# Performance work log

Measured on AMD Instinct MI355X. Metric: run time of the kernel, lower is better.

The kernel has to match this reference:

```python
import jax, jax.numpy as jnp
import numpy as np

N = 1_000_000
D = 128
S = 16384


def setup_inputs() -> dict:
    key = jax.random.key(0)
    k_x, k_idx, k_w, k_b = jax.random.split(key, 4)
    x = jax.random.normal(k_x, (N, D), dtype=jnp.float32)
    index = jnp.sort(jax.random.randint(k_idx, (N,), 0, S, dtype=jnp.int64))
    # single plain Linear layer of PyG MLP([D, D], plain_last=True)
    lim = 1.0 / np.sqrt(D)
    W = jax.random.uniform(k_w, (D, D), dtype=jnp.float32, minval=-lim, maxval=lim)
    b = jax.random.uniform(k_b, (D,), dtype=jnp.float32, minval=-lim, maxval=lim)
    return {"x": x, "W": W, "b": b, "index": index, "num_segments": S}


def reference(x, W, b, index, num_segments):
    # att = MLP(x): single plain linear layer (no activation, plain_last=True)
    att = x @ W.T + b  # [N, D]
    # segment softmax over nodes within each graph, per channel (PyG softmax)
    seg_max = jax.ops.segment_max(att, index, num_segments=num_segments)  # [S, D]
    e = jnp.exp(att - seg_max[index])  # [N, D]
    seg_sum = jax.ops.segment_sum(e, index, num_segments=num_segments)  # [S, D]
    att = e / (seg_sum[index] + 1e-16)  # [N, D]
    # attention-weighted global add pool
    return jax.ops.segment_sum(x * att, index, num_segments=num_segments)  # [S, D]
```

## Files before the change

### kernel.cpp

```cpp
#include <hip/hip_runtime.h>
#include <hip/hip_bf16.h>

#define SEGS   16384
#define DCH    128
#define CHUNK  32
#define SEGPB  4
#define FPITCH 132
#define XHBLK  520
#define LOG2E  1.4426950408889634f

using f32x4  = __attribute__((ext_vector_type(4))) float;
using bf16x8 = __attribute__((ext_vector_type(8))) short;
using u32x2  = __attribute__((ext_vector_type(2))) unsigned int;
using u32x4  = __attribute__((ext_vector_type(4))) unsigned int;

__device__ __forceinline__ float u2f(unsigned int u) { return __uint_as_float(u); }
__device__ __forceinline__ unsigned int f2u(float f) { return __float_as_uint(f); }

__global__ void setup_kernel(const float* __restrict__ W,
                             const int* __restrict__ index, int N,
                             unsigned short* __restrict__ WfH,
                             int* __restrict__ seg_start) {
  int i = blockIdx.x * blockDim.x + threadIdx.x;
  if (i < DCH * DCH) {
    int n = i >> 7, k = i & 127;
    float w = W[i] * LOG2E;
    unsigned int u = f2u(w);
    unsigned int r = (u + 0x7FFFu + ((u >> 16) & 1)) >> 16;
    int kt    = k >> 5;
    int ntile = n >> 4;
    int lane  = (n & 15) + 16 * ((k >> 3) & 3);
    int j     = k & 7;
    int dst = ((kt * 8 + ntile) * 64 + lane) * 8 + j;
    WfH[dst] = (unsigned short)r;
  } else if (i < DCH * DCH + SEGS + 1) {
    int s = i - DCH * DCH;
    int lo = 0, hi = N;
    while (lo < hi) {
      int mid = (lo + hi) >> 1;
      if (index[mid] < s) lo = mid + 1; else hi = mid;
    }
    seg_start[s] = lo;
  }
}

__global__ __launch_bounds__(256) void pool_kernel(
    const float* __restrict__ x, const float* __restrict__ bias,
    const int* __restrict__ seg_start,
    const u32x4* __restrict__ WfH,
    float* __restrict__ out) {
  __shared__ unsigned short xh[8 * XHBLK];
  __shared__ float          xf[CHUNK * FPITCH];

  const int t    = threadIdx.x;
  const int wv   = t >> 6;
  const int lane = t & 63;
  const int cl   = lane & 15;
  const int g    = lane >> 4;
  const int k31  = t & 31;
  const int lrow = t >> 5;
  const int lcol = k31 << 2;

  const int xh_base = 1040 * (k31 >> 3) + 8 * lrow + 128 * ((k31 >> 1) & 3) + 4 * (k31 & 1);
  const int xf_base = lrow * FPITCH + lcol;
  const int frag_base = lane * 8;
  const int ex_base   = g * 4 * FPITCH + wv * 32 + cl;

  u32x4 bh[4][2];
#pragma unroll
  for (int kt = 0; kt < 4; ++kt)
#pragma unroll
    for (int nt = 0; nt < 2; ++nt) {
      int off = (kt * 8 + (wv * 2 + nt)) * 64 + lane;
      bh[kt][nt] = WfH[off];
    }

  const float bc0 = bias[wv * 32 + cl]      * LOG2E;
  const float bc1 = bias[wv * 32 + 16 + cl] * LOG2E;

  const int s0   = blockIdx.x * SEGPB;
  const int sEnd = s0 + SEGPB;

  for (int es = s0; es < sEnd; ++es) {
    if (seg_start[es + 1] == seg_start[es] && lane < 16) {
      out[(size_t)es * DCH + wv * 32 + cl]      = 0.f;
      out[(size_t)es * DCH + wv * 32 + 16 + cl] = 0.f;
    }
  }

  int s = s0;
  while (s < sEnd && seg_start[s + 1] == seg_start[s]) ++s;
  if (s >= sEnd) return;

  int c0  = 0;
  int len = seg_start[s + 1] - seg_start[s];
  int cnt = (len < CHUNK) ? len : CHUNK;

  f32x4 pv[4];
  {
    const int base = seg_start[s];
#pragma unroll
    for (int p = 0; p < 4; ++p) {
      int lr = lrow + p * 8;
      f32x4 v = {0.f, 0.f, 0.f, 0.f};
      if (lr < cnt) v = *(const f32x4*)(x + (size_t)(base + lr) * DCH + lcol);
      pv[p] = v;
    }
  }

  float den[2] = {0.f, 0.f};
  float num[2] = {0.f, 0.f};

  while (true) {
    int ns = s, nc0 = c0 + CHUNK;
    if (nc0 >= len) {
      nc0 = 0; ns = s + 1;
      while (ns < sEnd && seg_start[ns + 1] == seg_start[ns]) ++ns;
    }
    const bool have_next = (ns < sEnd);
    int nlen = 0, ncnt = 0, nbase = 0;
    if (have_next) {
      nbase = seg_start[ns] + nc0;
      nlen  = seg_start[ns + 1] - seg_start[ns];
      ncnt  = nlen - nc0; if (ncnt > CHUNK) ncnt = CHUNK;
    }

#pragma unroll
    for (int p = 0; p < 4; ++p) {
      f32x4 v = pv[p];
      unsigned int u0 = f2u(v[0]), u1 = f2u(v[1]), u2 = f2u(v[2]), u3 = f2u(v[3]);
      u32x2 H = { (u1 & 0xFFFF0000u) | (u0 >> 16),
                  (u3 & 0xFFFF0000u) | (u2 >> 16) };
      *(u32x2*)&xh[xh_base + (p >> 1) * XHBLK + (p & 1) * 64] = H;
      *(f32x4*)&xf[xf_base + p * 8 * FPITCH] = v;
    }

    if (have_next) {
#pragma unroll
      for (int p = 0; p < 4; ++p) {
        int lr = lrow + p * 8;
        f32x4 v = {0.f, 0.f, 0.f, 0.f};
        if (lr < ncnt) v = *(const f32x4*)(x + (size_t)(nbase + lr) * DCH + lcol);
        pv[p] = v;
      }
    }

    asm volatile("s_waitcnt lgkmcnt(0)" ::: "memory");
    __builtin_amdgcn_sched_barrier(0);
    __builtin_amdgcn_s_barrier();
    __builtin_amdgcn_sched_barrier(0);

    f32x4 Cf[2][2];
#pragma unroll
    for (int mt = 0; mt < 2; ++mt) {
      Cf[mt][0] = (f32x4){bc0, bc0, bc0, bc0};
      Cf[mt][1] = (f32x4){bc1, bc1, bc1, bc1};
    }

#pragma unroll
    for (int kt = 0; kt < 4; ++kt) {
      u32x4 ah[2];
#pragma unroll
      for (int mt = 0; mt < 2; ++mt)
        ah[mt] = *(const u32x4*)&xh[frag_base + (2 * kt + mt) * XHBLK];
#pragma unroll
      for (int mt = 0; mt < 2; ++mt)
#pragma unroll
        for (int nt = 0; nt < 2; ++nt) {
          bf16x8 A = __builtin_bit_cast(bf16x8, ah[mt]);
          bf16x8 B = __builtin_bit_cast(bf16x8, bh[kt][nt]);
          Cf[mt][nt] = __builtin_amdgcn_mfma_f32_16x16x32_bf16(A, B, Cf[mt][nt], 0, 0, 0);
        }
    }

#pragma unroll
    for (int nt = 0; nt < 2; ++nt) {
#pragma unroll
      for (int mt = 0; mt < 2; ++mt)
#pragma unroll
        for (int r = 0; r < 4; ++r) {
          const int row = mt * 16 + g * 4 + r;
          float p = __builtin_amdgcn_exp2f(Cf[mt][nt][r]);
          p = (row < cnt) ? p : 0.f;
          float xv = xf[ex_base + (mt * 16 + r) * FPITCH + nt * 16];
          den[nt] += p;
          num[nt] += p * xv;
        }
    }

    if (c0 + CHUNK >= len) {
#pragma unroll
      for (int nt = 0; nt < 2; ++nt) {
        float l = den[nt], a = num[nt];
        l += __shfl_xor(l, 16); l += __shfl_xor(l, 32);
        a += __shfl_xor(a, 16); a += __shfl_xor(a, 32);
        if (lane < 16)
          out[(size_t)s * DCH + wv * 32 + nt * 16 + cl] = a / (l + 1e-16f);
        den[nt] = 0.f; num[nt] = 0.f;
      }
      if (!have_next) break;
      s = ns; len = nlen; c0 = 0;
    } else {
      c0 = nc0;
    }
    cnt = ncnt;

    asm volatile("s_waitcnt lgkmcnt(0)" ::: "memory");
    __builtin_amdgcn_sched_barrier(0);
    __builtin_amdgcn_s_barrier();
    __builtin_amdgcn_sched_barrier(0);
  }
}

extern "C" void kernel_launch(void* const* d_in, const int* in_sizes, int n_in,
                              void* d_out, int out_size, void* d_ws, size_t ws_size,
                              hipStream_t stream) {
  const float* x    = (const float*)d_in[0];
  const float* W    = (const float*)d_in[1];
  const float* bias = (const float*)d_in[2];
  const int*   idx  = (const int*)d_in[3];
  const int N = in_sizes[0] / DCH;

  unsigned short* WfH = (unsigned short*)d_ws;
  int* seg = (int*)(WfH + DCH * DCH);

  int setup_threads = DCH * DCH + SEGS + 1;
  setup_kernel<<<(setup_threads + 255) / 256, 256, 0, stream>>>(W, idx, N, WfH, seg);
  pool_kernel<<<SEGS / SEGPB, 256, 0, stream>>>(x, bias, seg,
                                                (const u32x4*)WfH,
                                                (float*)d_out);
}
```

Before: 125.1 us.

## Deepen x prefetch to two chunks ahead and double segments per block

Register prefetch of x chunks moves from one chunk ahead to two, using ping-pong buffers pvA/pvB. Each chunk's load is issued two iterations before it is consumed, which gives more time to hide global memory latency. SEGPB also doubles from 4 to 8, so the grid has half as many blocks, each handling more segments. The cost is higher register pressure and fewer blocks, which may reduce occupancy and parallelism.

After: 129.9 us. +3.8%, slower.

```diff
diff --git a/kernel.cpp b/kernel.cpp
--- a/kernel.cpp
+++ b/kernel.cpp
@@ -4,7 +4,7 @@
 #define SEGS   16384
 #define DCH    128
 #define CHUNK  32
-#define SEGPB  4
+#define SEGPB  8
 #define FPITCH 132
 #define XHBLK  520
 #define LOG2E  1.4426950408889634f
@@ -92,13 +92,13 @@
   while (s < sEnd && seg_start[s + 1] == seg_start[s]) ++s;
   if (s >= sEnd) return;
 
-  int c0  = 0;
-  int len = seg_start[s + 1] - seg_start[s];
-  int cnt = (len < CHUNK) ? len : CHUNK;
-
-  f32x4 pv[4];
-  {
-    const int base = seg_start[s];
+  int curS = s, curC0 = 0;
+  int curLen = seg_start[s + 1] - seg_start[s];
+  int curCnt = (curLen < CHUNK) ? curLen : CHUNK;
+
+  f32x4 pvA[4], pvB[4];
+
+  auto issue = [&](f32x4 (&pv)[4], int base, int cnt) {
 #pragma unroll
     for (int p = 0; p < 4; ++p) {
       int lr = lrow + p * 8;
@@ -106,28 +106,37 @@
       if (lr < cnt) v = *(const f32x4*)(x + (size_t)(base + lr) * DCH + lcol);
       pv[p] = v;
     }
-  }
+  };
+
+  issue(pvA, seg_start[s], curCnt);
+
+  auto adv = [&](int fs, int fc0, int flen,
+                 int &os, int &oc0, int &olen, int &ocnt, int &obase) -> bool {
+    int ns = fs, nc = fc0 + CHUNK;
+    if (nc >= flen) {
+      nc = 0; ns = fs + 1;
+      while (ns < sEnd && seg_start[ns + 1] == seg_start[ns]) ++ns;
+    }
+    if (ns >= sEnd) return false;
+    int st = seg_start[ns];
+    os = ns; oc0 = nc; olen = seg_start[ns + 1] - st;
+    ocnt = olen - nc; if (ocnt > CHUNK) ocnt = CHUNK;
+    obase = st + nc;
+    return true;
+  };
+
+  int nxtS = 0, nxtC0 = 0, nxtLen = 0, nxtCnt = 0, nxtBase = 0;
+  bool nxtV = adv(curS, curC0, curLen, nxtS, nxtC0, nxtLen, nxtCnt, nxtBase);
+  if (nxtV) issue(pvB, nxtBase, nxtCnt);
 
   float den[2] = {0.f, 0.f};
   float num[2] = {0.f, 0.f};
 
-  while (true) {
-    int ns = s, nc0 = c0 + CHUNK;
-    if (nc0 >= len) {
-      nc0 = 0; ns = s + 1;
-      while (ns < sEnd && seg_start[ns + 1] == seg_start[ns]) ++ns;
-    }
-    const bool have_next = (ns < sEnd);
-    int nlen = 0, ncnt = 0, nbase = 0;
-    if (have_next) {
-      nbase = seg_start[ns] + nc0;
-      nlen  = seg_start[ns + 1] - seg_start[ns];
-      ncnt  = nlen - nc0; if (ncnt > CHUNK) ncnt = CHUNK;
-    }
-
+  auto body = [&](f32x4 (&pvS)[4], f32x4 (&pvL)[4]) -> bool {
+    (void)pvL;
 #pragma unroll
     for (int p = 0; p < 4; ++p) {
-      f32x4 v = pv[p];
+      f32x4 v = pvS[p];
       unsigned int u0 = f2u(v[0]), u1 = f2u(v[1]), u2 = f2u(v[2]), u3 = f2u(v[3]);
       u32x2 H = { (u1 & 0xFFFF0000u) | (u0 >> 16),
                   (u3 & 0xFFFF0000u) | (u2 >> 16) };
@@ -135,14 +144,11 @@
       *(f32x4*)&xf[xf_base + p * 8 * FPITCH] = v;
     }
 
-    if (have_next) {
-#pragma unroll
-      for (int p = 0; p < 4; ++p) {
-        int lr = lrow + p * 8;
-        f32x4 v = {0.f, 0.f, 0.f, 0.f};
-        if (lr < ncnt) v = *(const f32x4*)(x + (size_t)(nbase + lr) * DCH + lcol);
-        pv[p] = v;
-      }
+    int nnS = 0, nnC0 = 0, nnLen = 0, nnCnt = 0, nnBase = 0;
+    bool nnV = false;
+    if (nxtV) {
+      nnV = adv(nxtS, nxtC0, nxtLen, nnS, nnC0, nnLen, nnCnt, nnBase);
+      if (nnV) issue(pvS, nnBase, nnCnt);
     }
 
     asm volatile("s_waitcnt lgkmcnt(0)" ::: "memory");
@@ -156,7 +162,6 @@
       Cf[mt][0] = (f32x4){bc0, bc0, bc0, bc0};
       Cf[mt][1] = (f32x4){bc1, bc1, bc1, bc1};
     }
-
 #pragma unroll
     for (int kt = 0; kt < 4; ++kt) {
       u32x4 ah[2];
@@ -181,34 +186,39 @@
         for (int r = 0; r < 4; ++r) {
           const int row = mt * 16 + g * 4 + r;
           float p = __builtin_amdgcn_exp2f(Cf[mt][nt][r]);
-          p = (row < cnt) ? p : 0.f;
+          p = (row < curCnt) ? p : 0.f;
           float xv = xf[ex_base + (mt * 16 + r) * FPITCH + nt * 16];
           den[nt] += p;
           num[nt] += p * xv;
         }
     }
 
-    if (c0 + CHUNK >= len) {
+    if (curC0 + CHUNK >= curLen) {
 #pragma unroll
       for (int nt = 0; nt < 2; ++nt) {
         float l = den[nt], a = num[nt];
         l += __shfl_xor(l, 16); l += __shfl_xor(l, 32);
         a += __shfl_xor(a, 16); a += __shfl_xor(a, 32);
         if (lane < 16)
-          out[(size_t)s * DCH + wv * 32 + nt * 16 + cl] = a / (l + 1e-16f);
+          out[(size_t)curS * DCH + wv * 32 + nt * 16 + cl] = a / (l + 1e-16f);
         den[nt] = 0.f; num[nt] = 0.f;
       }
-      if (!have_next) break;
-      s = ns; len = nlen; c0 = 0;
-    } else {
-      c0 = nc0;
-    }
-    cnt = ncnt;
+    }
+    if (!nxtV) return false;
+    curS = nxtS; curC0 = nxtC0; curLen = nxtLen; curCnt = nxtCnt;
+    nxtS = nnS; nxtC0 = nnC0; nxtLen = nnLen; nxtCnt = nnCnt; nxtBase = nnBase;
+    nxtV = nnV;
 
     asm volatile("s_waitcnt lgkmcnt(0)" ::: "memory");
     __builtin_amdgcn_sched_barrier(0);
     __builtin_amdgcn_s_barrier();
     __builtin_amdgcn_sched_barrier(0);
+    return true;
+  };
+
+  for (;;) {
+    if (!body(pvA, pvB)) break;
+    if (!body(pvB, pvA)) break;
   }
 }
 
```

## Pack rows of all block segments contiguously into chunks instead of per-segment chunks

Applied to the files above, without the earlier changes.

Instead of processing each segment in its own 32-row chunks (padding partial chunks), the block now streams the contiguous row range spanning its four segments in full 32-row chunks. Rows of several segments share one MFMA tile, and masking by segment boundaries splits the accumulation. Since segments average about 61 rows, this cuts wasted MFMA and load work on partially filled chunks. The cost is a segment-boundary loop with repeated masked accumulation passes per chunk.

Measured after the change: 119.3 us. 1.05x faster.

```diff
diff --git a/kernel.cpp b/kernel.cpp
--- a/kernel.cpp
+++ b/kernel.cpp
@@ -80,51 +80,36 @@
 
   const int s0   = blockIdx.x * SEGPB;
   const int sEnd = s0 + SEGPB;
-
-  for (int es = s0; es < sEnd; ++es) {
-    if (seg_start[es + 1] == seg_start[es] && lane < 16) {
-      out[(size_t)es * DCH + wv * 32 + cl]      = 0.f;
-      out[(size_t)es * DCH + wv * 32 + 16 + cl] = 0.f;
-    }
-  }
-
-  int s = s0;
-  while (s < sEnd && seg_start[s + 1] == seg_start[s]) ++s;
-  if (s >= sEnd) return;
-
-  int c0  = 0;
-  int len = seg_start[s + 1] - seg_start[s];
-  int cnt = (len < CHUNK) ? len : CHUNK;
-
+  const int R0   = seg_start[s0];
+  const int R1   = seg_start[sEnd];
+
+  if (R0 == R1) {
+    if (lane < 16) {
+      for (int es = s0; es < sEnd; ++es) {
+        out[(size_t)es * DCH + wv * 32 + cl]      = 0.f;
+        out[(size_t)es * DCH + wv * 32 + 16 + cl] = 0.f;
+      }
+    }
+    return;
+  }
+
+  int curSeg = s0;
+  int segEnd = seg_start[curSeg + 1];
+
+  int c0 = R0;
   f32x4 pv[4];
-  {
-    const int base = seg_start[s];
-#pragma unroll
-    for (int p = 0; p < 4; ++p) {
-      int lr = lrow + p * 8;
-      f32x4 v = {0.f, 0.f, 0.f, 0.f};
-      if (lr < cnt) v = *(const f32x4*)(x + (size_t)(base + lr) * DCH + lcol);
-      pv[p] = v;
-    }
+#pragma unroll
+  for (int p = 0; p < 4; ++p) {
+    int lr = c0 + lrow + p * 8;
+    f32x4 v = {0.f, 0.f, 0.f, 0.f};
+    if (lr < R1) v = *(const f32x4*)(x + (size_t)lr * DCH + lcol);
+    pv[p] = v;
   }
 
   float den[2] = {0.f, 0.f};
   float num[2] = {0.f, 0.f};
 
   while (true) {
-    int ns = s, nc0 = c0 + CHUNK;
-    if (nc0 >= len) {
-      nc0 = 0; ns = s + 1;
-      while (ns < sEnd && seg_start[ns + 1] == seg_start[ns]) ++ns;
-    }
-    const bool have_next = (ns < sEnd);
-    int nlen = 0, ncnt = 0, nbase = 0;
-    if (have_next) {
-      nbase = seg_start[ns] + nc0;
-      nlen  = seg_start[ns + 1] - seg_start[ns];
-      ncnt  = nlen - nc0; if (ncnt > CHUNK) ncnt = CHUNK;
-    }
-
 #pragma unroll
     for (int p = 0; p < 4; ++p) {
       f32x4 v = pv[p];
@@ -135,12 +120,13 @@
       *(f32x4*)&xf[xf_base + p * 8 * FPITCH] = v;
     }
 
-    if (have_next) {
+    const int nc0 = c0 + CHUNK;
+    if (nc0 < R1) {
 #pragma unroll
       for (int p = 0; p < 4; ++p) {
-        int lr = lrow + p * 8;
+        int lr = nc0 + lrow + p * 8;
         f32x4 v = {0.f, 0.f, 0.f, 0.f};
-        if (lr < ncnt) v = *(const f32x4*)(x + (size_t)(nbase + lr) * DCH + lcol);
+        if (lr < R1) v = *(const f32x4*)(x + (size_t)lr * DCH + lcol);
         pv[p] = v;
       }
     }
@@ -156,7 +142,6 @@
       Cf[mt][0] = (f32x4){bc0, bc0, bc0, bc0};
       Cf[mt][1] = (f32x4){bc1, bc1, bc1, bc1};
     }
-
 #pragma unroll
     for (int kt = 0; kt < 4; ++kt) {
       u32x4 ah[2];
@@ -173,37 +158,53 @@
         }
     }
 
-#pragma unroll
-    for (int nt = 0; nt < 2; ++nt) {
+    float pr[2][2][4], xv[2][2][4];
+#pragma unroll
+    for (int nt = 0; nt < 2; ++nt)
 #pragma unroll
       for (int mt = 0; mt < 2; ++mt)
 #pragma unroll
         for (int r = 0; r < 4; ++r) {
-          const int row = mt * 16 + g * 4 + r;
-          float p = __builtin_amdgcn_exp2f(Cf[mt][nt][r]);
-          p = (row < cnt) ? p : 0.f;
-          float xv = xf[ex_base + (mt * 16 + r) * FPITCH + nt * 16];
-          den[nt] += p;
-          num[nt] += p * xv;
+          pr[nt][mt][r] = __builtin_amdgcn_exp2f(Cf[mt][nt][r]);
+          xv[nt][mt][r] = xf[ex_base + (mt * 16 + r) * FPITCH + nt * 16];
         }
-    }
-
-    if (c0 + CHUNK >= len) {
-#pragma unroll
-      for (int nt = 0; nt < 2; ++nt) {
-        float l = den[nt], a = num[nt];
-        l += __shfl_xor(l, 16); l += __shfl_xor(l, 32);
-        a += __shfl_xor(a, 16); a += __shfl_xor(a, 32);
-        if (lane < 16)
-          out[(size_t)s * DCH + wv * 32 + nt * 16 + cl] = a / (l + 1e-16f);
-        den[nt] = 0.f; num[nt] = 0.f;
+
+    const int lim = c0 + CHUNK;
+    int lo = c0;
+    while (curSeg < sEnd) {
+      const int hi  = segEnd;
+      const int hiC = (hi < lim) ? hi : lim;
+#pragma unroll
+      for (int nt = 0; nt < 2; ++nt)
+#pragma unroll
+        for (int mt = 0; mt < 2; ++mt)
+#pragma unroll
+          for (int r = 0; r < 4; ++r) {
+            const int row = c0 + mt * 16 + g * 4 + r;
+            const bool use = (row >= lo) & (row < hiC);
+            const float pp = use ? pr[nt][mt][r] : 0.f;
+            den[nt] += pp;
+            num[nt] += pp * xv[nt][mt][r];
+          }
+      if (hi <= lim) {
+#pragma unroll
+        for (int nt = 0; nt < 2; ++nt) {
+          float l = den[nt], a = num[nt];
+          l += __shfl_xor(l, 16); l += __shfl_xor(l, 32);
+          a += __shfl_xor(a, 16); a += __shfl_xor(a, 32);
+          if (lane < 16)
+            out[(size_t)curSeg * DCH + wv * 32 + nt * 16 + cl] = a / (l + 1e-16f);
+          den[nt] = 0.f; num[nt] = 0.f;
+        }
+        lo = hi;
+        ++curSeg;
+        if (curSeg < sEnd) segEnd = seg_start[curSeg + 1];
+      } else {
+        break;
       }
-      if (!have_next) break;
-      s = ns; len = nlen; c0 = 0;
-    } else {
-      c0 = nc0;
-    }
-    cnt = ncnt;
+    }
+    if (curSeg >= sEnd) break;
+    c0 = nc0;
 
     asm volatile("s_waitcnt lgkmcnt(0)" ::: "memory");
     __builtin_amdgcn_sched_barrier(0);
```
